# Optimization experiments

Measured on AMD Instinct MI355X. Metric: run time of the kernel, lower is better.

The kernel has to match this reference:

```python
import jax, jax.numpy as jnp
import numpy as np

NUM_HEADS = 8
NEG_MASK = -1000.0  # original code masks with -1000, not -inf


def setup_inputs() -> dict:
    key = jax.random.key(0)
    ks = jax.random.split(key, 12)
    B, S, D = 4, 2048, 512
    HID, OUT = 512, 512
    dh = D // NUM_HEADS      # 64, per-head input dim
    eh = HID // NUM_HEADS    # 64, per-head hidden dim
    w = 0.02
    return {
        "q": jax.random.normal(ks[0], (B, S, D), dtype=jnp.float32),
        "k": jax.random.normal(ks[1], (B, S, D), dtype=jnp.float32),
        "v": jax.random.normal(ks[2], (B, S, D), dtype=jnp.float32),
        # Linear weights stored as [in, out] (transpose of torch convention)
        "Wq": jax.random.normal(ks[3], (dh, eh), dtype=jnp.float32) * w,
        "bq": jax.random.normal(ks[4], (eh,), dtype=jnp.float32) * w,
        "Wk": jax.random.normal(ks[5], (dh, eh), dtype=jnp.float32) * w,
        "bk": jax.random.normal(ks[6], (eh,), dtype=jnp.float32) * w,
        "Wv": jax.random.normal(ks[7], (dh, eh), dtype=jnp.float32) * w,
        "bv": jax.random.normal(ks[8], (eh,), dtype=jnp.float32) * w,
        "Wo": jax.random.normal(ks[9], (HID, OUT), dtype=jnp.float32) * w,
        "bo": jax.random.normal(ks[10], (OUT,), dtype=jnp.float32) * w,
        "valid_lens": jnp.maximum(jax.random.randint(ks[11], (B,), 0, S), 1),
        "max_len": S,
    }


def reference(q, k, v, Wq, bq, Wk, bk, Wv, bv, Wo, bo, valid_lens, max_len):
    B, S, D = q.shape
    H = NUM_HEADS
    # split into heads: [B, S, H, dh]; note the SAME projection weights are
    # shared across heads (as in the original module)
    qh = q.reshape(B, S, H, D // H)
    kh = k.reshape(B, S, H, D // H)
    vh = v.reshape(B, S, H, D // H)
    qp = jnp.einsum('bshd,de->bshe', qh, Wq) + bq  # [B,S,H,eh]
    kp = jnp.einsum('bshd,de->bshe', kh, Wk) + bk
    vp = jnp.einsum('bshd,de->bshe', vh, Wv) + bv
    scale = 1.0 / jnp.sqrt(jnp.asarray(qp.shape[-1], qp.dtype))
    scores = jnp.einsum('bshe,bthe->bhst', qp, kp) * scale  # [B,H,S,S]
    # key-padding mask: positions j >= valid_len get -1000 (original semantics)
    key_mask = jnp.arange(S)[None, :] < valid_lens[:, None]  # [B,S]
    scores = jnp.where(key_mask[:, None, None, :], scores, NEG_MASK)
    attn = jax.nn.softmax(scores, axis=-1)
    ctx = jnp.einsum('bhst,bthe->bshe', attn, vp).reshape(B, S, -1)  # head-major concat
    return jnp.einsum('bse,eo->bso', ctx, Wo) + bo
```

## Files before the change

kernel.cpp:

```cpp
#include <hip/hip_runtime.h>

#define S_LEN 2048
#define D_MODEL 512

typedef __attribute__((ext_vector_type(8))) short s8v;
typedef __attribute__((ext_vector_type(4))) float f4v;
typedef __attribute__((ext_vector_type(4))) short s4v;
typedef __attribute__((ext_vector_type(4))) int   i4v;
typedef __attribute__((ext_vector_type(2))) int   i2v;

#define MFMA __builtin_amdgcn_mfma_f32_16x16x32_bf16

__device__ inline short f2bf(float x) {
    union { float f; unsigned u; } v; v.f = x;
    unsigned r = v.u + 0x7fffu + ((v.u >> 16) & 1u);
    return (short)(r >> 16);
}
__device__ inline unsigned pack_bf2_trunc(float a, float b) {
    unsigned ua = __builtin_bit_cast(unsigned, a);
    unsigned ub = __builtin_bit_cast(unsigned, b);
    return (ua >> 16) | (ub & 0xffff0000u);
}

template <int C>
__device__ inline float dppf(float x) {
    int i = __builtin_bit_cast(int, x);
    i = __builtin_amdgcn_update_dpp(0, i, C, 0xF, 0xF, true);
    return __builtin_bit_cast(float, i);
}
__device__ inline float rowsum16(float x) {
    x += dppf<0xB1>(x);
    x += dppf<0x4E>(x);
    x += dppf<0x141>(x);
    x += dppf<0x140>(x);
    return x;
}

__global__ __launch_bounds__(256) void prep_kernel(
    const float* __restrict__ Wo, const float* __restrict__ Wq,
    const float* __restrict__ Wk, const float* __restrict__ Wv,
    short* __restrict__ WoT, short* __restrict__ WqT,
    short* __restrict__ WkT, short* __restrict__ WvT)
{
    if (blockIdx.x < 64) {
        __shared__ short t[64 * 65];
        const int bi = (blockIdx.x >> 3) * 64;
        const int bj = (blockIdx.x & 7) * 64;
        const int c = threadIdx.x & 63, rr = threadIdx.x >> 6;
#pragma unroll
        for (int r = 0; r < 16; r++) {
            int i = r * 4 + rr;
            t[c * 65 + i] = f2bf(Wo[(size_t)(bi + i) * 512 + bj + c]);
        }
        __syncthreads();
#pragma unroll
        for (int r = 0; r < 16; r++) {
            int o = r * 4 + rr;
            WoT[(size_t)(bj + o) * 512 + bi + c] = t[o * 65 + c];
        }
    } else {
        for (int j = threadIdx.x; j < 12288; j += 256) {
            int w = j >> 12, r = j & 4095;
            int e = r >> 6, d = r & 63;
            const float* W = (w == 0) ? Wq : (w == 1) ? Wk : Wv;
            short* WT = (w == 0) ? WqT : (w == 1) ? WkT : WvT;
            WT[r] = f2bf(W[d * 64 + e]);
        }
    }
}

__global__ __launch_bounds__(256) void proj_kernel(
    const float* __restrict__ q, const float* __restrict__ k, const float* __restrict__ v,
    const float* __restrict__ bq, const float* __restrict__ bk, const float* __restrict__ bv,
    const short* __restrict__ WqT, const short* __restrict__ WkT, const short* __restrict__ WvT,
    short* __restrict__ qp, short* __restrict__ kp, short* __restrict__ vpT)
{
    const int t = blockIdx.z >> 2;
    const int b = blockIdx.z & 3;
    const int h = blockIdx.y;
    const int qt = blockIdx.x;
    const int w = threadIdx.x >> 6, lane = threadIdx.x & 63;
    const int l = lane & 15, qd = lane >> 4;

    const float* X    = (t == 0) ? q   : (t == 1) ? k   : v;
    const float* bias = (t == 0) ? bq  : (t == 1) ? bk  : bv;
    const short* WT   = (t == 0) ? WqT : (t == 1) ? WkT : WvT;

    const int s0 = qt * 128 + w * 32;

    s8v a[2][2];
#pragma unroll
    for (int mt = 0; mt < 2; mt++)
#pragma unroll
        for (int kk = 0; kk < 2; kk++) {
            const float* p = X + (size_t)(b * S_LEN + s0 + mt * 16 + l) * 512 + h * 64 + kk * 32 + qd * 8;
            f4v x0 = *(const f4v*)p;
            f4v x1 = *(const f4v*)(p + 4);
            s8v fr;
            fr[0] = f2bf(x0[0]); fr[1] = f2bf(x0[1]); fr[2] = f2bf(x0[2]); fr[3] = f2bf(x0[3]);
            fr[4] = f2bf(x1[0]); fr[5] = f2bf(x1[1]); fr[6] = f2bf(x1[2]); fr[7] = f2bf(x1[3]);
            a[mt][kk] = fr;
        }
    s8v wf[4][2];
#pragma unroll
    for (int nt = 0; nt < 4; nt++) {
        int wrow = (t < 2) ? (4 * l + nt) : (nt * 16 + l);
#pragma unroll
        for (int kk = 0; kk < 2; kk++)
            wf[nt][kk] = *(const s8v*)(WT + wrow * 64 + kk * 32 + qd * 8);
    }

    const f4v fz = {0.f, 0.f, 0.f, 0.f};
    f4v acc[2][4];
#pragma unroll
    for (int mt = 0; mt < 2; mt++)
#pragma unroll
        for (int nt = 0; nt < 4; nt++) acc[mt][nt] = fz;

#pragma unroll
    for (int kk = 0; kk < 2; kk++)
#pragma unroll
        for (int nt = 0; nt < 4; nt++)
#pragma unroll
            for (int mt = 0; mt < 2; mt++)
                acc[mt][nt] = MFMA(a[mt][kk], wf[nt][kk], acc[mt][nt], 0, 0, 0);

    const float SC = 0.125f * 1.442695041f;

    if (t < 2) {
        short* out = (t == 0) ? qp : kp;
        float bbs[4];
#pragma unroll
        for (int nt = 0; nt < 4; nt++) bbs[nt] = bias[4 * l + nt];
#pragma unroll
        for (int mt = 0; mt < 2; mt++)
#pragma unroll
            for (int r = 0; r < 4; r++) {
                int s = s0 + mt * 16 + qd * 4 + r;
                s4v pk;
#pragma unroll
                for (int nt = 0; nt < 4; nt++) {
                    float val = acc[mt][nt][r] + bbs[nt];
                    if (t == 0) val *= SC;
                    pk[nt] = f2bf(val);
                }
                *(s4v*)(out + ((size_t)(b * 8 + h) * S_LEN + s) * 64 + 4 * l) = pk;
            }
    } else {
#pragma unroll
        for (int nt = 0; nt < 4; nt++) {
            float bb = bias[nt * 16 + l];
            int e = nt * 16 + l;
#pragma unroll
            for (int mt = 0; mt < 2; mt++) {
                s4v pk;
#pragma unroll
                for (int r = 0; r < 4; r++) pk[r] = f2bf(acc[mt][nt][r] + bb);
                *(s4v*)(vpT + ((size_t)(b * 8 + h) * 64 + e) * S_LEN + s0 + mt * 16 + qd * 4) = pk;
            }
        }
    }
}

__global__ __launch_bounds__(128) void repack_kernel(
    const short* __restrict__ kp, const short* __restrict__ vpT,
    short* __restrict__ kfrag, short* __restrict__ vfrag)
{
    const int kb = blockIdx.x, h = blockIdx.y, b = blockIdx.z;
    const int bh = b * 8 + h;
    const int half = threadIdx.x >> 6, f = threadIdx.x & 63;
    const int l = f & 15, qd = f >> 4;
    const size_t slab = (size_t)bh * S_LEN * 64;
    const size_t obase = ((size_t)bh * 32 + kb) * 4096;
    if (half == 0) {
        const short* src = kp + slab;
#pragma unroll
        for (int c = 0; c < 8; c++) {
            int nt = c >> 1, kk = c & 1;
            s8v x = *(const s8v*)(src + (size_t)(kb * 64 + 4 * l + nt) * 64 + kk * 32 + qd * 8);
            *(s8v*)(kfrag + obase + c * 512 + f * 8) = x;
        }
    } else {
        const short* src = vpT + slab;
#pragma unroll
        for (int c = 0; c < 8; c++) {
            int ne = c >> 1, kk = c & 1;
            s8v x = *(const s8v*)(src + (size_t)(4 * l + ne) * S_LEN + kb * 64 + kk * 32 + qd * 8);
            *(s8v*)(vfrag + obase + c * 512 + f * 8) = x;
        }
    }
}

__global__ __launch_bounds__(128) void attn_kernel(
    const short* __restrict__ qp, const short* __restrict__ kfrag,
    const short* __restrict__ vfrag,
    const int* __restrict__ valid_lens, short* __restrict__ ctx)
{
    __shared__ short lP[2][32 * 72];

    const int gid = blockIdx.x;
    const int h  = gid & 7;
    const int b  = (gid >> 3) & 3;
    const int qt = gid >> 5;
    const int w = threadIdx.x >> 6, lane = threadIdx.x & 63;
    const int l = lane & 15, qd = lane >> 4;
    const int vlen = valid_lens[b];
    const int ntiles = (vlen + 63) >> 6;

    const int bh = b * 8 + h;
    const short* Qs = qp + (size_t)bh * S_LEN * 64;
    const short* Kf = kfrag + (size_t)bh * 32 * 4096;
    const short* Vf = vfrag + (size_t)bh * 32 * 4096;

    const int s0 = qt * 64 + w * 32;
    s8v qf[2][2];
#pragma unroll
    for (int mt = 0; mt < 2; mt++)
#pragma unroll
        for (int kk = 0; kk < 2; kk++)
            qf[mt][kk] = *(const s8v*)(Qs + (size_t)(s0 + mt * 16 + l) * 64 + kk * 32 + qd * 8);

    const f4v fz = {0.f, 0.f, 0.f, 0.f};
    f4v O[2][4];
    float lsum[2][4];
#pragma unroll
    for (int mt = 0; mt < 2; mt++)
#pragma unroll
        for (int r = 0; r < 4; r++) lsum[mt][r] = 0.f;
#pragma unroll
    for (int mt = 0; mt < 2; mt++)
#pragma unroll
        for (int ne = 0; ne < 4; ne++) O[mt][ne] = fz;

    short* lPw = lP[w];

    for (int kb = 0; kb < ntiles; kb++) {
        const short* Kb = Kf + (size_t)kb * 4096 + lane * 8;
        s8v kf[4][2];
#pragma unroll
        for (int nt = 0; nt < 4; nt++)
#pragma unroll
            for (int kk = 0; kk < 2; kk++)
                kf[nt][kk] = *(const s8v*)(Kb + (nt * 2 + kk) * 512);

        f4v sf[2][4];
#pragma unroll
        for (int mt = 0; mt < 2; mt++)
#pragma unroll
            for (int nt = 0; nt < 4; nt++) sf[mt][nt] = fz;
#pragma unroll
        for (int nt = 0; nt < 4; nt++)
#pragma unroll
            for (int mt = 0; mt < 2; mt++) {
                sf[mt][nt] = MFMA(qf[mt][0], kf[nt][0], sf[mt][nt], 0, 0, 0);
                sf[mt][nt] = MFMA(qf[mt][1], kf[nt][1], sf[mt][nt], 0, 0, 0);
            }

        const short* Vb = Vf + (size_t)kb * 4096 + lane * 8;
        s8v vf[4][2];
#pragma unroll
        for (int ne = 0; ne < 4; ne++)
#pragma unroll
            for (int kk = 0; kk < 2; kk++)
                vf[ne][kk] = *(const s8v*)(Vb + (ne * 2 + kk) * 512);

        if (kb == ntiles - 1 && (vlen & 63)) {
            int rem = vlen - kb * 64;
#pragma unroll
            for (int nt = 0; nt < 4; nt++)
                if (4 * l + nt >= rem) {
#pragma unroll
                    for (int mt = 0; mt < 2; mt++)
#pragma unroll
                        for (int r = 0; r < 4; r++) sf[mt][nt][r] = -1e30f;
                }
        }

#pragma unroll
        for (int mt = 0; mt < 2; mt++)
#pragma unroll
            for (int r = 0; r < 4; r++) {
                float p0 = __builtin_amdgcn_exp2f(sf[mt][0][r]);
                float p1 = __builtin_amdgcn_exp2f(sf[mt][1][r]);
                float p2 = __builtin_amdgcn_exp2f(sf[mt][2][r]);
                float p3 = __builtin_amdgcn_exp2f(sf[mt][3][r]);
                lsum[mt][r] += (p0 + p1) + (p2 + p3);
                i2v pk;
                pk[0] = (int)pack_bf2_trunc(p0, p1);
                pk[1] = (int)pack_bf2_trunc(p2, p3);
                *(i2v*)(lPw + (mt * 16 + qd * 4 + r) * 72 + 4 * l) = pk;
            }

        s8v pa[2][2];
#pragma unroll
        for (int mt = 0; mt < 2; mt++)
#pragma unroll
            for (int kk = 0; kk < 2; kk++)
                pa[mt][kk] = *(const s8v*)(lPw + (mt * 16 + l) * 72 + kk * 32 + qd * 8);
#pragma unroll
        for (int ne = 0; ne < 4; ne++)
#pragma unroll
            for (int mt = 0; mt < 2; mt++) {
                O[mt][ne] = MFMA(pa[mt][0], vf[ne][0], O[mt][ne], 0, 0, 0);
                O[mt][ne] = MFMA(pa[mt][1], vf[ne][1], O[mt][ne], 0, 0, 0);
            }
    }

#pragma unroll
    for (int mt = 0; mt < 2; mt++)
#pragma unroll
        for (int r = 0; r < 4; r++) {
            float inv = 1.0f / rowsum16(lsum[mt][r]);
            int s = s0 + mt * 16 + qd * 4 + r;
            s4v pk;
#pragma unroll
            for (int ne = 0; ne < 4; ne++) pk[ne] = f2bf(O[mt][ne][r] * inv);
            *(s4v*)(ctx + ((size_t)(b * S_LEN + s)) * 512 + h * 64 + 4 * l) = pk;
        }
}

__global__ __launch_bounds__(256) void outproj_kernel(
    const short* __restrict__ ctx, const short* __restrict__ WoT,
    const float* __restrict__ bo, float* __restrict__ out)
{
    __shared__ short lB[64 * 520];
    __shared__ short lA[128 * 40];

    const int rb = blockIdx.x * 128;
    const int nb = blockIdx.y * 64;
    const int w = threadIdx.x >> 6, lane = threadIdx.x & 63;
    const int l = lane & 15, qd = lane >> 4;

    {
        int n = threadIdx.x >> 2, c0 = threadIdx.x & 3;
#pragma unroll
        for (int i = 0; i < 16; i++) {
            int g = i * 4 + c0;
            i4v x = *(const i4v*)(WoT + (size_t)(nb + n) * 512 + g * 8);
            *(i4v*)(lB + n * 520 + g * 8) = x;
        }
    }
    __syncthreads();

    const f4v fz = {0.f, 0.f, 0.f, 0.f};
    f4v acc[2][4];
#pragma unroll
    for (int mt = 0; mt < 2; mt++)
#pragma unroll
        for (int nt = 0; nt < 4; nt++) acc[mt][nt] = fz;

    for (int ko = 0; ko < 16; ko++) {
        {
            int r = threadIdx.x >> 1, hp = threadIdx.x & 1;
            const short* src = ctx + (size_t)(rb + r) * 512 + ko * 32 + hp * 16;
            i4v x0 = *(const i4v*)src;
            i4v x1 = *(const i4v*)(src + 8);
            *(i4v*)(lA + r * 40 + hp * 16) = x0;
            *(i4v*)(lA + r * 40 + hp * 16 + 8) = x1;
        }
        __syncthreads();
        s8v af[2];
#pragma unroll
        for (int mt = 0; mt < 2; mt++)
            af[mt] = *(const s8v*)(lA + (w * 32 + mt * 16 + l) * 40 + qd * 8);
#pragma unroll
        for (int nt = 0; nt < 4; nt++) {
            s8v bfr = *(const s8v*)(lB + (nt * 16 + l) * 520 + ko * 32 + qd * 8);
#pragma unroll
            for (int mt = 0; mt < 2; mt++)
                acc[mt][nt] = MFMA(af[mt], bfr, acc[mt][nt], 0, 0, 0);
        }
        __syncthreads();
    }

#pragma unroll
    for (int nt = 0; nt < 4; nt++) {
        float bias = bo[nb + nt * 16 + l];
#pragma unroll
        for (int mt = 0; mt < 2; mt++)
#pragma unroll
            for (int r = 0; r < 4; r++) {
                int row = rb + w * 32 + mt * 16 + qd * 4 + r;
                out[(size_t)row * 512 + nb + nt * 16 + l] = acc[mt][nt][r] + bias;
            }
    }
}

extern "C" void kernel_launch(void* const* d_in, const int* in_sizes, int n_in,
                              void* d_out, int out_size, void* d_ws, size_t ws_size,
                              hipStream_t stream)
{
    const float* q  = (const float*)d_in[0];
    const float* k  = (const float*)d_in[1];
    const float* v  = (const float*)d_in[2];
    const float* Wq = (const float*)d_in[3];
    const float* bq = (const float*)d_in[4];
    const float* Wk = (const float*)d_in[5];
    const float* bk = (const float*)d_in[6];
    const float* Wv = (const float*)d_in[7];
    const float* bv = (const float*)d_in[8];
    const float* Wo = (const float*)d_in[9];
    const float* bo = (const float*)d_in[10];
    const int*   vl = (const int*)d_in[11];
    float* out = (float*)d_out;

    char* ws = (char*)d_ws;
    const size_t SL = (size_t)4 * 8 * S_LEN * 64 * sizeof(short);
    short* qp    = (short*)(ws);
    short* kp    = (short*)(ws + SL);
    short* ctx   = (short*)(ws + SL);
    short* vpT   = (short*)(ws + 2 * SL);
    short* kfrag = (short*)(ws + 3 * SL);
    short* vfrag = (short*)(ws + 4 * SL);
    short* WoT = (short*)(ws + 5 * SL);
    short* WqT = WoT + 512 * 512;
    short* WkT = WqT + 4096;
    short* WvT = WkT + 4096;

    prep_kernel<<<65, 256, 0, stream>>>(Wo, Wq, Wk, Wv, WoT, WqT, WkT, WvT);
    proj_kernel<<<dim3(16, 8, 12), 256, 0, stream>>>(q, k, v, bq, bk, bv,
                                                     WqT, WkT, WvT, qp, kp, vpT);
    repack_kernel<<<dim3(32, 8, 4), 128, 0, stream>>>(kp, vpT, kfrag, vfrag);
    attn_kernel<<<1024, 128, 0, stream>>>(qp, kfrag, vfrag, vl, ctx);
    outproj_kernel<<<dim3(64, 8), 256, 0, stream>>>(ctx, WoT, bo, out);
}
```

Measured before the change: 193.9 us.

## Split attention key tiles across two waves per row group and merge partials

Doubles the attention block to four waves, where each pair of waves processes alternating key tiles for the same 32 query rows. The odd wave writes its partial O accumulators and row sums to shared memory, and the even wave adds them before normalizing and storing ctx. This is meant to shorten the serial key loop per wave and raise occupancy. The cost is the extra shared-memory reduction, two block barriers and higher register pressure per block.

```diff
diff --git a/kernel.cpp b/kernel.cpp
--- a/kernel.cpp
+++ b/kernel.cpp
@@ -191,18 +191,21 @@
     }
 }
 
-__global__ __launch_bounds__(128) void attn_kernel(
+__global__ __launch_bounds__(256) void attn_kernel(
     const short* __restrict__ qp, const short* __restrict__ kfrag,
     const short* __restrict__ vfrag,
     const int* __restrict__ valid_lens, short* __restrict__ ctx)
 {
-    __shared__ short lP[2][32 * 72];
+    __shared__ long long lmem[2624];
 
     const int gid = blockIdx.x;
     const int h  = gid & 7;
     const int b  = (gid >> 3) & 3;
     const int qt = gid >> 5;
-    const int w = threadIdx.x >> 6, lane = threadIdx.x & 63;
+    const int wv = threadIdx.x >> 6;
+    const int rg = wv >> 1;
+    const int par = wv & 1;
+    const int lane = threadIdx.x & 63;
     const int l = lane & 15, qd = lane >> 4;
     const int vlen = valid_lens[b];
     const int ntiles = (vlen + 63) >> 6;
@@ -212,7 +215,7 @@
     const short* Kf = kfrag + (size_t)bh * 32 * 4096;
     const short* Vf = vfrag + (size_t)bh * 32 * 4096;
 
-    const int s0 = qt * 64 + w * 32;
+    const int s0 = qt * 64 + rg * 32;
     s8v qf[2][2];
 #pragma unroll
     for (int mt = 0; mt < 2; mt++)
@@ -232,9 +235,9 @@
 #pragma unroll
         for (int ne = 0; ne < 4; ne++) O[mt][ne] = fz;
 
-    short* lPw = lP[w];
-
-    for (int kb = 0; kb < ntiles; kb++) {
+    short* lPw = (short*)lmem + wv * 32 * 72;
+
+    for (int kb = par; kb < ntiles; kb += 2) {
         const short* Kb = Kf + (size_t)kb * 4096 + lane * 8;
         s8v kf[4][2];
 #pragma unroll
@@ -306,17 +309,47 @@
             }
     }
 
-#pragma unroll
-    for (int mt = 0; mt < 2; mt++)
-#pragma unroll
-        for (int r = 0; r < 4; r++) {
-            float inv = 1.0f / rowsum16(lsum[mt][r]);
-            int s = s0 + mt * 16 + qd * 4 + r;
-            s4v pk;
-#pragma unroll
-            for (int ne = 0; ne < 4; ne++) pk[ne] = f2bf(O[mt][ne][r] * inv);
-            *(s4v*)(ctx + ((size_t)(b * S_LEN + s)) * 512 + h * 64 + 4 * l) = pk;
-        }
+    __syncthreads();
+    float* fbuf = (float*)lmem;
+    if (par == 1) {
+        float* dst = fbuf + (rg * 64 + lane) * 41;
+#pragma unroll
+        for (int mt = 0; mt < 2; mt++)
+#pragma unroll
+            for (int ne = 0; ne < 4; ne++)
+#pragma unroll
+                for (int r = 0; r < 4; r++) dst[(mt * 4 + ne) * 4 + r] = O[mt][ne][r];
+#pragma unroll
+        for (int mt = 0; mt < 2; mt++)
+#pragma unroll
+            for (int r = 0; r < 4; r++) dst[32 + mt * 4 + r] = lsum[mt][r];
+    }
+    __syncthreads();
+    if (par == 0) {
+        const float* src = fbuf + (rg * 64 + lane) * 41;
+#pragma unroll
+        for (int mt = 0; mt < 2; mt++)
+#pragma unroll
+            for (int ne = 0; ne < 4; ne++)
+#pragma unroll
+                for (int r = 0; r < 4; r++) O[mt][ne][r] += src[(mt * 4 + ne) * 4 + r];
+#pragma unroll
+        for (int mt = 0; mt < 2; mt++)
+#pragma unroll
+            for (int r = 0; r < 4; r++) lsum[mt][r] += src[32 + mt * 4 + r];
+
+#pragma unroll
+        for (int mt = 0; mt < 2; mt++)
+#pragma unroll
+            for (int r = 0; r < 4; r++) {
+                float inv = 1.0f / rowsum16(lsum[mt][r]);
+                int s = s0 + mt * 16 + qd * 4 + r;
+                s4v pk;
+#pragma unroll
+                for (int ne = 0; ne < 4; ne++) pk[ne] = f2bf(O[mt][ne][r] * inv);
+                *(s4v*)(ctx + ((size_t)(b * S_LEN + s)) * 512 + h * 64 + 4 * l) = pk;
+            }
+    }
 }
 
 __global__ __launch_bounds__(256) void outproj_kernel(
@@ -421,6 +454,6 @@
     proj_kernel<<<dim3(16, 8, 12), 256, 0, stream>>>(q, k, v, bq, bk, bv,
                                                      WqT, WkT, WvT, qp, kp, vpT);
     repack_kernel<<<dim3(32, 8, 4), 128, 0, stream>>>(kp, vpT, kfrag, vfrag);
-    attn_kernel<<<1024, 128, 0, stream>>>(qp, kfrag, vfrag, vl, ctx);
+    attn_kernel<<<1024, 256, 0, stream>>>(qp, kfrag, vfrag, vl, ctx);
     outproj_kernel<<<dim3(64, 8), 256, 0, stream>>>(ctx, WoT, bo, out);
 }
```

Result: no change. 194.3 us (+0.2%).

## Share K/V tiles across four waves via double-buffered async LDS staging

Applied to the files above, without the earlier changes.

The attention kernel now runs 256-thread blocks covering 128 query rows, so there are four waves per block instead of two, and the grid halves to 512 blocks. Each K/V tile is loaded from global memory into a double-buffered LDS buffer with global_load_lds, and the next tile is prefetched while the current one is computed. This aims to cut redundant global K/V traffic and hide load latency. The cost is a block-wide barrier every iteration, more LDS per block, and fewer blocks for a 256-CU part.

```diff
diff --git a/kernel.cpp b/kernel.cpp
--- a/kernel.cpp
+++ b/kernel.cpp
@@ -191,18 +191,20 @@
     }
 }
 
-__global__ __launch_bounds__(128) void attn_kernel(
+__global__ __launch_bounds__(256) void attn_kernel(
     const short* __restrict__ qp, const short* __restrict__ kfrag,
     const short* __restrict__ vfrag,
     const int* __restrict__ valid_lens, short* __restrict__ ctx)
 {
-    __shared__ short lP[2][32 * 72];
+    __shared__ short lKV[2][8192];
+    __shared__ short lP[4 * 32 * 72];
 
     const int gid = blockIdx.x;
     const int h  = gid & 7;
     const int b  = (gid >> 3) & 3;
     const int qt = gid >> 5;
-    const int w = threadIdx.x >> 6, lane = threadIdx.x & 63;
+    const int wv = threadIdx.x >> 6;
+    const int lane = threadIdx.x & 63;
     const int l = lane & 15, qd = lane >> 4;
     const int vlen = valid_lens[b];
     const int ntiles = (vlen + 63) >> 6;
@@ -212,7 +214,7 @@
     const short* Kf = kfrag + (size_t)bh * 32 * 4096;
     const short* Vf = vfrag + (size_t)bh * 32 * 4096;
 
-    const int s0 = qt * 64 + w * 32;
+    const int s0 = qt * 128 + wv * 32;
     s8v qf[2][2];
 #pragma unroll
     for (int mt = 0; mt < 2; mt++)
@@ -232,16 +234,37 @@
 #pragma unroll
         for (int ne = 0; ne < 4; ne++) O[mt][ne] = fz;
 
-    short* lPw = lP[w];
-
+    short* lPw = lP + wv * 32 * 72;
+
+    auto stage = [&](int kb, int buf) {
+#pragma unroll
+        for (int c = 0; c < 4; c++) {
+            int j = wv * 4 + c;
+            const short* src = (j < 8)
+                ? Kf + (size_t)kb * 4096 + j * 512 + lane * 8
+                : Vf + (size_t)kb * 4096 + (j - 8) * 512 + lane * 8;
+            short* dst = &lKV[buf][j * 512];
+            __builtin_amdgcn_global_load_lds(
+                (const __attribute__((address_space(1))) unsigned int*)src,
+                (__attribute__((address_space(3))) unsigned int*)dst, 16, 0, 0);
+        }
+    };
+
+    stage(0, 0);
     for (int kb = 0; kb < ntiles; kb++) {
-        const short* Kb = Kf + (size_t)kb * 4096 + lane * 8;
+        const int buf = kb & 1;
+        __syncthreads();
+        if (kb + 1 < ntiles) stage(kb + 1, buf ^ 1);
+
+        const short* lK = lKV[buf];
+        const short* lV = lKV[buf] + 4096;
+
         s8v kf[4][2];
 #pragma unroll
         for (int nt = 0; nt < 4; nt++)
 #pragma unroll
             for (int kk = 0; kk < 2; kk++)
-                kf[nt][kk] = *(const s8v*)(Kb + (nt * 2 + kk) * 512);
+                kf[nt][kk] = *(const s8v*)(lK + (nt * 2 + kk) * 512 + lane * 8);
 
         f4v sf[2][4];
 #pragma unroll
@@ -256,13 +279,12 @@
                 sf[mt][nt] = MFMA(qf[mt][1], kf[nt][1], sf[mt][nt], 0, 0, 0);
             }
 
-        const short* Vb = Vf + (size_t)kb * 4096 + lane * 8;
         s8v vf[4][2];
 #pragma unroll
         for (int ne = 0; ne < 4; ne++)
 #pragma unroll
             for (int kk = 0; kk < 2; kk++)
-                vf[ne][kk] = *(const s8v*)(Vb + (ne * 2 + kk) * 512);
+                vf[ne][kk] = *(const s8v*)(lV + (ne * 2 + kk) * 512 + lane * 8);
 
         if (kb == ntiles - 1 && (vlen & 63)) {
             int rem = vlen - kb * 64;
@@ -421,6 +443,6 @@
     proj_kernel<<<dim3(16, 8, 12), 256, 0, stream>>>(q, k, v, bq, bk, bv,
                                                      WqT, WkT, WvT, qp, kp, vpT);
     repack_kernel<<<dim3(32, 8, 4), 128, 0, stream>>>(kp, vpT, kfrag, vfrag);
-    attn_kernel<<<1024, 128, 0, stream>>>(qp, kfrag, vfrag, vl, ctx);
+    attn_kernel<<<512, 256, 0, stream>>>(qp, kfrag, vfrag, vl, ctx);
     outproj_kernel<<<dim3(64, 8), 256, 0, stream>>>(ctx, WoT, bo, out);
 }
```

New measurement: 196.6 us. No clear change (+1.4%).
